# Kernel tuning notes

Measured on AMD Instinct MI355X. Metric: run time of the kernel, lower is better.

The kernel has to match this reference:

```python
import jax, jax.numpy as jnp
import numpy as np

HEADS = 4
DIM_HEAD = 32
GROUPS = 32  # min(256//4, 32)
EPS = 1e-5


def setup_inputs() -> dict:
    key = jax.random.key(0)
    ks = jax.random.split(key, 5)
    B, C, H, W = 16, 256, 64, 64
    CD, HC, WC = 512, 32, 32
    hid = HEADS * DIM_HEAD  # 128
    return {
        "x": jax.random.normal(ks[0], (B, C, H, W), jnp.float32),
        "cond": jax.random.normal(ks[1], (B, CD, HC, WC), jnp.float32),
        "gn_w": jnp.ones((C,), jnp.float32),
        "gn_b": jnp.zeros((C,), jnp.float32),
        "w_q": jax.random.normal(ks[2], (hid, C), jnp.float32) * 0.05,
        "b_q": jnp.zeros((hid,), jnp.float32),
        "w_kv": jax.random.normal(ks[3], (2 * hid, CD), jnp.float32) * 0.05,
        "b_kv": jnp.zeros((2 * hid,), jnp.float32),
        "w_out": jax.random.normal(ks[4], (C, hid), jnp.float32) * 0.05,
        "b_out": jnp.zeros((C,), jnp.float32),
    }


def _group_norm(x, w, b):
    # x: (B, C, H, W); normalize per group over (channels-in-group, H, W)
    B, C, H, W = x.shape
    xg = x.reshape(B, GROUPS, C // GROUPS, H, W)
    mu = jnp.mean(xg, axis=(2, 3, 4), keepdims=True)
    var = jnp.var(xg, axis=(2, 3, 4), keepdims=True)
    xn = ((xg - mu) * jax.lax.rsqrt(var + EPS)).reshape(B, C, H, W)
    return xn * w[None, :, None, None] + b[None, :, None, None]


def _conv1x1(x, w, b):
    # x: (B, Cin, H, W), w: (Cout, Cin), b: (Cout,)
    return jnp.einsum('oc,bchw->bohw', w, x) + b[None, :, None, None]


def reference(x, cond, gn_w, gn_b, w_q, b_q, w_kv, b_kv, w_out, b_out):
    B, C, H, W = x.shape
    hid = HEADS * DIM_HEAD
    xn = _group_norm(x, gn_w, gn_b)
    q = _conv1x1(xn, w_q, b_q)          # (B, hid, H, W)
    kv = _conv1x1(cond, w_kv, b_kv)     # (B, 2*hid, Hc, Wc)
    Nc = kv.shape[2] * kv.shape[3]
    N = H * W
    k = kv[:, :hid].reshape(B, HEADS, DIM_HEAD, Nc)
    v = kv[:, hid:].reshape(B, HEADS, DIM_HEAD, Nc)
    q = q.reshape(B, HEADS, DIM_HEAD, N)
    k = jax.nn.softmax(k, axis=-1)
    # kv outer product: (B, heads, d, e)
    context = jnp.einsum('bhdn,bhen->bhde', k, v)
    # query contraction over d: (B, heads, e, n)
    out = jnp.einsum('bhde,bhdn->bhen', context, q)
    out = out.reshape(B, hid, H, W)
    return _conv1x1(out, w_out, b_out)
```

## Files before the change

kernel.cpp:

```cpp
#include <hip/hip_runtime.h>
#include <hip/hip_bf16.h>

typedef __attribute__((ext_vector_type(8))) short bf16x8;
typedef __attribute__((ext_vector_type(4))) float f32x4;

__device__ __forceinline__ ushort f2bf(float f) {
    __hip_bfloat16 h = __float2bfloat16(f);
    return __builtin_bit_cast(ushort, h);
}
__device__ __forceinline__ unsigned pack2(float a, float b) {
    return (unsigned)f2bf(a) | ((unsigned)f2bf(b) << 16);
}
__device__ __forceinline__ float bflo(unsigned u) { return __uint_as_float(u << 16); }
__device__ __forceinline__ float bfhi(unsigned u) { return __uint_as_float(u & 0xffff0000u); }

__device__ __forceinline__ void unpack8(uint4 r, float* o) {
    o[0] = bflo(r.x); o[1] = bfhi(r.x); o[2] = bflo(r.y); o[3] = bfhi(r.y);
    o[4] = bflo(r.z); o[5] = bfhi(r.z); o[6] = bflo(r.w); o[7] = bfhi(r.w);
}

__global__ __launch_bounds__(256) void kv_gemm(const float* __restrict__ w_kv,
                                               const float* __restrict__ cond,
                                               const float* __restrict__ b_kv,
                                               ushort* __restrict__ kv16,
                                               float* __restrict__ zbase) {
    __shared__ ushort lA[128 * 64];
    __shared__ ushort lB[32 * 64];
    __shared__ float scratch[64 * 32];
    int nc = blockIdx.x, rb = blockIdx.y, b = blockIdx.z;
    int t = threadIdx.x;
    int fid = blockIdx.x + 32 * (blockIdx.y + 2 * blockIdx.z);
    if (fid < 264) zbase[fid * 256 + t] = 0.f;
    int col0 = nc * 32, row0 = rb * 128;
    int l = t & 63, w = t >> 6;
    int lr = l & 15, lg = l >> 4;
    const float* Ab32 = w_kv + (size_t)row0 * 512;
    const float* Bb = cond + (size_t)b * 512 * 1024 + col0;
    int rA = t >> 3, gAr = t & 7, gw = gAr ^ (rA & 7);
    int rB = t >> 3, gB = t & 7;
    int sp = t & 31, sj4 = (t >> 5) & 7;
    float4 ka0_, ka1_, ka2_, ka3_, ka4_, ka5_, ka6_, ka7_;
    float4 kb0_, kb1_;
#define KG_LOADA(k0) { \
    ka0_ = *(const float4*)&Ab32[(size_t)(rA)      * 512 + (k0) + gAr * 8]; \
    ka1_ = *(const float4*)&Ab32[(size_t)(rA)      * 512 + (k0) + gAr * 8 + 4]; \
    ka2_ = *(const float4*)&Ab32[(size_t)(32 + rA) * 512 + (k0) + gAr * 8]; \
    ka3_ = *(const float4*)&Ab32[(size_t)(32 + rA) * 512 + (k0) + gAr * 8 + 4]; \
    ka4_ = *(const float4*)&Ab32[(size_t)(64 + rA) * 512 + (k0) + gAr * 8]; \
    ka5_ = *(const float4*)&Ab32[(size_t)(64 + rA) * 512 + (k0) + gAr * 8 + 4]; \
    ka6_ = *(const float4*)&Ab32[(size_t)(96 + rA) * 512 + (k0) + gAr * 8]; \
    ka7_ = *(const float4*)&Ab32[(size_t)(96 + rA) * 512 + (k0) + gAr * 8 + 4]; }
#define KG_LOADB(k0) { \
    kb0_ = *(const float4*)&Bb[(size_t)((k0) + rB)      * 1024 + gB * 4]; \
    kb1_ = *(const float4*)&Bb[(size_t)((k0) + 32 + rB) * 1024 + gB * 4]; }
#define KG_WRITEA() { uint4 p; \
    p.x = pack2(ka0_.x, ka0_.y); p.y = pack2(ka0_.z, ka0_.w); \
    p.z = pack2(ka1_.x, ka1_.y); p.w = pack2(ka1_.z, ka1_.w); \
    *(uint4*)((char*)lA + (size_t)((rA)      * 8 + gw) * 16) = p; \
    p.x = pack2(ka2_.x, ka2_.y); p.y = pack2(ka2_.z, ka2_.w); \
    p.z = pack2(ka3_.x, ka3_.y); p.w = pack2(ka3_.z, ka3_.w); \
    *(uint4*)((char*)lA + (size_t)((32 + rA) * 8 + gw) * 16) = p; \
    p.x = pack2(ka4_.x, ka4_.y); p.y = pack2(ka4_.z, ka4_.w); \
    p.z = pack2(ka5_.x, ka5_.y); p.w = pack2(ka5_.z, ka5_.w); \
    *(uint4*)((char*)lA + (size_t)((64 + rA) * 8 + gw) * 16) = p; \
    p.x = pack2(ka6_.x, ka6_.y); p.y = pack2(ka6_.z, ka6_.w); \
    p.z = pack2(ka7_.x, ka7_.y); p.w = pack2(ka7_.z, ka7_.w); \
    *(uint4*)((char*)lA + (size_t)((96 + rA) * 8 + gw) * 16) = p; }
#define KG_WRITEB() { \
    *(float4*)((char*)scratch + (rB)      * 128 + ((gB ^ (((rB)      >> 1) & 7)) * 16)) = kb0_; \
    *(float4*)((char*)scratch + (32 + rB) * 128 + ((gB ^ (((32 + rB) >> 1) & 7)) * 16)) = kb1_; }
#define KG_PACKB() { \
    int js = sj4 ^ (sp & 7); \
    float4 s0 = *(const float4*)((char*)scratch + (2*sp)   * 128 + js * 16); \
    float4 s2 = *(const float4*)((char*)scratch + (2*sp+1) * 128 + js * 16); \
    float c0v[4] = {s0.x, s0.y, s0.z, s0.w}; \
    float c1v[4] = {s2.x, s2.y, s2.z, s2.w}; \
    _Pragma("unroll") \
    for (int w4 = 0; w4 < 4; ++w4) { \
        int n = sj4 * 4 + w4; \
        unsigned pk = pack2(c0v[w4], c1v[w4]); \
        *(unsigned*)((char*)lB + n * 128 + (((sp >> 2) ^ (n & 7)) * 16) + (sp & 3) * 4) = pk; \
    } }
    KG_LOADA(0); KG_LOADB(0);
    f32x4 acc[2][2] = {};
    for (int it = 0; it < 8; ++it) {
        KG_WRITEA();
        KG_WRITEB();
        __syncthreads();
        if (it < 7) { KG_LOADA(it * 64 + 64); KG_LOADB(it * 64 + 64); }
        KG_PACKB();
        __syncthreads();
        __builtin_amdgcn_s_setprio(1);
        #pragma unroll
        for (int ks = 0; ks < 2; ++ks) {
            bf16x8 av[2], bv[2];
            #pragma unroll
            for (int mi = 0; mi < 2; ++mi) {
                int ar = w * 32 + mi * 16 + lr;
                int q = (ks * 4 + lg) ^ (ar & 7);
                av[mi] = *(const bf16x8*)((const char*)lA + ar * 128 + q * 16);
            }
            #pragma unroll
            for (int ni = 0; ni < 2; ++ni) {
                int br = ni * 16 + lr;
                int q = (ks * 4 + lg) ^ (br & 7);
                bv[ni] = *(const bf16x8*)((const char*)lB + br * 128 + q * 16);
            }
            #pragma unroll
            for (int mi = 0; mi < 2; ++mi)
                #pragma unroll
                for (int ni = 0; ni < 2; ++ni)
                    acc[mi][ni] = __builtin_amdgcn_mfma_f32_16x16x32_bf16(
                        av[mi], bv[ni], acc[mi][ni], 0, 0, 0);
        }
        __builtin_amdgcn_s_setprio(0);
        __syncthreads();
    }
#undef KG_LOADA
#undef KG_LOADB
#undef KG_WRITEA
#undef KG_WRITEB
#undef KG_PACKB
    int orow = row0 + w * 32;
    #pragma unroll
    for (int mi = 0; mi < 2; ++mi) {
        int rbase = orow + mi * 16 + lg * 4;
        float4 b4 = *(const float4*)&b_kv[rbase];
        float bvr[4] = {b4.x, b4.y, b4.z, b4.w};
        #pragma unroll
        for (int ni = 0; ni < 2; ++ni) {
            int cc = col0 + ni * 16 + lr;
            #pragma unroll
            for (int r = 0; r < 4; ++r)
                kv16[((size_t)b * 256 + rbase + r) * 1024 + cc] = f2bf(acc[mi][ni][r] + bvr[r]);
        }
    }
}

__global__ __launch_bounds__(256) void ctxstats_kernel(const ushort* __restrict__ kv,
                                                       const float* __restrict__ x,
                                                       float* __restrict__ rowsum,
                                                       float* __restrict__ ctx,
                                                       float* __restrict__ statacc) {
    __shared__ float pl[32][129], vl[32][129];
    int bid = blockIdx.x, t = threadIdx.x;
    if (bid < 512) {
        int bh = bid >> 3, b = bh >> 2, h = bh & 3;
        int n0 = (bid & 7) * 128;
        int r = t >> 3, cs = (t & 7) * 16;
        const ushort* kp = kv + ((size_t)b * 256 + h * 32 + r) * 1024 + n0 + cs;
        const ushort* vp = kv + ((size_t)b * 256 + 128 + h * 32 + r) * 1024 + n0 + cs;
        float kvals[16], vvals[16];
        unpack8(((const uint4*)kp)[0], kvals);
        unpack8(((const uint4*)kp)[1], kvals + 8);
        unpack8(((const uint4*)vp)[0], vvals);
        unpack8(((const uint4*)vp)[1], vvals + 8);
        float psum = 0.f;
        #pragma unroll
        for (int i = 0; i < 16; ++i) {
            float e = __expf(kvals[i]);
            pl[r][cs + i] = e;
            vl[r][cs + i] = vvals[i];
            psum += e;
        }
        psum += __shfl_xor(psum, 1, 64);
        psum += __shfl_xor(psum, 2, 64);
        psum += __shfl_xor(psum, 4, 64);
        if ((t & 7) == 0) atomicAdd(&rowsum[bh * 32 + r], psum);
        __syncthreads();
        int d0 = t >> 5, e0 = t & 31;
        float acc[4] = {0.f, 0.f, 0.f, 0.f};
        #pragma unroll 8
        for (int nn = 0; nn < 128; ++nn) {
            float vv = vl[e0][nn];
            #pragma unroll
            for (int i = 0; i < 4; ++i)
                acc[i] += pl[d0 + 8 * i][nn] * vv;
        }
        #pragma unroll
        for (int i = 0; i < 4; ++i)
            atomicAdd(&ctx[((size_t)bh * 32 + d0 + 8 * i) * 32 + e0], acc[i]);
    } else {
        int bg = bid - 512;
        const float4* xp = (const float4*)(x + (size_t)bg * 32768);
        float s = 0.f, ss = 0.f;
        #pragma unroll
        for (int j = 0; j < 32; ++j) {
            float4 v = xp[t + 256 * j];
            s  += v.x + v.y + v.z + v.w;
            ss += v.x*v.x + v.y*v.y + v.z*v.z + v.w*v.w;
        }
        #pragma unroll
        for (int off = 32; off > 0; off >>= 1) {
            s  += __shfl_down(s, off, 64);
            ss += __shfl_down(ss, off, 64);
        }
        int wave = t >> 6;
        if ((t & 63) == 0) { pl[0][wave * 2] = s; pl[0][wave * 2 + 1] = ss; }
        __syncthreads();
        if (t == 0) {
            statacc[bg * 2]     = pl[0][0] + pl[0][2] + pl[0][4] + pl[0][6];
            statacc[bg * 2 + 1] = pl[0][1] + pl[0][3] + pl[0][5] + pl[0][7];
        }
    }
}

__global__ __launch_bounds__(256) void a_kernel(const float* __restrict__ ctx,
                                                const float* __restrict__ rowsum,
                                                const float* __restrict__ w_out,
                                                const float* __restrict__ w_q,
                                                const float* __restrict__ b_q,
                                                const float* __restrict__ b_out,
                                                ushort* __restrict__ A16,
                                                float* __restrict__ biasb) {
    __shared__ float ctxl[4][32][33];
    __shared__ float wol[16][128];
    __shared__ float ml[16][128];
    int b = blockIdx.x >> 4, ot = (blockIdx.x & 15) << 4;
    int t = threadIdx.x;
    #pragma unroll
    for (int j = 0; j < 16; ++j) {
        int e = t + 256 * j;
        float inv = 1.f / rowsum[b * 128 + (e >> 5)];
        ctxl[e >> 10][(e >> 5) & 31][e & 31] = ctx[(size_t)b * 4096 + e] * inv;
    }
    #pragma unroll
    for (int j = 0; j < 8; ++j) {
        int e = t + 256 * j;
        wol[e >> 7][e & 127] = w_out[(ot + (e >> 7)) * 128 + (e & 127)];
    }
    __syncthreads();
    #pragma unroll
    for (int j = 0; j < 8; ++j) {
        int e = t + 256 * j;
        int o = e >> 7, hd = e & 127, h = hd >> 5, d = hd & 31;
        float acc = 0.f;
        #pragma unroll
        for (int ee = 0; ee < 32; ++ee) acc += wol[o][h * 32 + ee] * ctxl[h][d][ee];
        ml[o][hd] = acc;
    }
    __syncthreads();
    int c = t;
    float wt[16];
    #pragma unroll
    for (int o = 0; o < 16; ++o) wt[o] = 0.f;
    for (int hd = 0; hd < 128; ++hd) {
        float wq = w_q[hd * 256 + c];
        #pragma unroll
        for (int o = 0; o < 16; ++o) wt[o] += ml[o][hd] * wq;
    }
    ushort* Abp = A16 + ((size_t)b * 256 + ot) * 256 + c;
    #pragma unroll
    for (int o = 0; o < 16; ++o)
        Abp[(size_t)o * 256] = f2bf(wt[o]);
    if (t < 16) {
        int o = t;
        float md = 0.f;
        #pragma unroll 8
        for (int hd = 0; hd < 128; ++hd) md += ml[o][hd] * b_q[hd];
        biasb[(size_t)b * 256 + ot + o] = md + b_out[ot + o];
    }
}

__global__ __launch_bounds__(512) void out_gemm_fused(const ushort* __restrict__ A16,
                                                      const float* __restrict__ x,
                                                      const float* __restrict__ statacc,
                                                      const float* __restrict__ gn_w,
                                                      const float* __restrict__ gn_b,
                                                      const float* __restrict__ biasb,
                                                      float* __restrict__ out) {
    __shared__ ushort lA[256 * 64];
    __shared__ ushort lB[64 * 64];
    __shared__ float scratch[64 * 64];
    __shared__ float sct[256][2];
    int b = blockIdx.y;
    int n0 = blockIdx.x * 64;
    int t = threadIdx.x;
    int l = t & 63, wid = t >> 6;
    int wr = wid >> 1, wc = wid & 1;
    int lr = l & 15, lg = l >> 4;
    const ushort* Ab = A16 + (size_t)b * 65536;
    const float* xb = x + (size_t)b * 256 * 4096 + n0;
    int sp = t & 31, sj4 = t >> 5;
    if (t < 256) {
        int g = t >> 3;
        float S  = statacc[(b * 32 + g) * 2];
        float SS = statacc[(b * 32 + g) * 2 + 1];
        float mu  = S * (1.f / 32768.f);
        float var = SS * (1.f / 32768.f) - mu * mu;
        float sc = rsqrtf(var + 1e-5f) * gn_w[t];
        sct[t][0] = sc;
        sct[t][1] = gn_b[t] - mu * sc;
    }
    uint4 a0_, a1_, a2_, a3_;
    float4 b0_, b1_;
    int rA = t >> 3, gA = (t & 7) ^ (rA & 7);
    int rB = t >> 4, gB = t & 15;
#define OG_LOADA(k0) { \
    a0_ = *(const uint4*)(Ab + (size_t)(rA)       * 256 + (k0) + gA * 8); \
    a1_ = *(const uint4*)(Ab + (size_t)(64 + rA)  * 256 + (k0) + gA * 8); \
    a2_ = *(const uint4*)(Ab + (size_t)(128 + rA) * 256 + (k0) + gA * 8); \
    a3_ = *(const uint4*)(Ab + (size_t)(192 + rA) * 256 + (k0) + gA * 8); }
#define OG_LOADB(k0) { \
    b0_ = *(const float4*)&xb[(size_t)((k0) + rB)      * 4096 + gB * 4]; \
    b1_ = *(const float4*)&xb[(size_t)((k0) + 32 + rB) * 4096 + gB * 4]; }
    OG_LOADA(0); OG_LOADB(0);
    f32x4 acc[4][2] = {};
    for (int it = 0; it < 4; ++it) {
        int k0 = it * 64;
        *(uint4*)((char*)lA + (size_t)t * 16)          = a0_;
        *(uint4*)((char*)lA + (size_t)(512 + t) * 16)  = a1_;
        *(uint4*)((char*)lA + (size_t)(1024 + t) * 16) = a2_;
        *(uint4*)((char*)lA + (size_t)(1536 + t) * 16) = a3_;
        *(float4*)((char*)scratch + (rB)      * 256 + ((gB ^ (((rB)      >> 1) & 15)) * 16)) = b0_;
        *(float4*)((char*)scratch + (32 + rB) * 256 + ((gB ^ (((32 + rB) >> 1) & 15)) * 16)) = b1_;
        __syncthreads();
        if (it < 3) { OG_LOADA(k0 + 64); OG_LOADB(k0 + 64); }
        {
            int js = sj4 ^ (sp & 15);
            float sc0 = sct[k0 + 2 * sp][0],     tc0 = sct[k0 + 2 * sp][1];
            float sc1 = sct[k0 + 2 * sp + 1][0], tc1 = sct[k0 + 2 * sp + 1][1];
            float4 s0 = *(const float4*)((char*)scratch + (2*sp)   * 256 + js * 16);
            float4 s2 = *(const float4*)((char*)scratch + (2*sp+1) * 256 + js * 16);
            float c0v[4] = {s0.x, s0.y, s0.z, s0.w};
            float c1v[4] = {s2.x, s2.y, s2.z, s2.w};
            #pragma unroll
            for (int w4 = 0; w4 < 4; ++w4) {
                int n = sj4 * 4 + w4;
                unsigned pk = pack2(c0v[w4] * sc0 + tc0, c1v[w4] * sc1 + tc1);
                *(unsigned*)((char*)lB + n * 128 + (((sp >> 2) ^ (n & 7)) * 16) + (sp & 3) * 4) = pk;
            }
        }
        __syncthreads();
        __builtin_amdgcn_s_setprio(1);
        #pragma unroll
        for (int ks = 0; ks < 2; ++ks) {
            bf16x8 av[4], bv[2];
            #pragma unroll
            for (int mi = 0; mi < 4; ++mi) {
                int ar = wr * 64 + mi * 16 + lr;
                int q = (ks * 4 + lg) ^ (ar & 7);
                av[mi] = *(const bf16x8*)((const char*)lA + ar * 128 + q * 16);
            }
            #pragma unroll
            for (int ni = 0; ni < 2; ++ni) {
                int br = wc * 32 + ni * 16 + lr;
                int q = (ks * 4 + lg) ^ (br & 7);
                bv[ni] = *(const bf16x8*)((const char*)lB + br * 128 + q * 16);
            }
            #pragma unroll
            for (int mi = 0; mi < 4; ++mi)
                #pragma unroll
                for (int ni = 0; ni < 2; ++ni)
                    acc[mi][ni] = __builtin_amdgcn_mfma_f32_16x16x32_bf16(
                        av[mi], bv[ni], acc[mi][ni], 0, 0, 0);
        }
        __builtin_amdgcn_s_setprio(0);
        __syncthreads();
    }
#undef OG_LOADA
#undef OG_LOADB
    const float* bp = biasb + (size_t)b * 256;
    int orow = wr * 64, ocol = n0 + wc * 32 + lr;
    #pragma unroll
    for (int mi = 0; mi < 4; ++mi) {
        int rb2 = orow + mi * 16 + lg * 4;
        float4 b4 = *(const float4*)&bp[rb2];
        float bvr[4] = {b4.x, b4.y, b4.z, b4.w};
        #pragma unroll
        for (int ni = 0; ni < 2; ++ni) {
            int cc = ocol + ni * 16;
            #pragma unroll
            for (int r = 0; r < 4; ++r)
                out[((size_t)b * 256 + rb2 + r) * 4096 + cc] = acc[mi][ni][r] + bvr[r];
        }
    }
}

extern "C" void kernel_launch(void* const* d_in, const int* in_sizes, int n_in,
                              void* d_out, int out_size, void* d_ws, size_t ws_size,
                              hipStream_t stream) {
    const float* x     = (const float*)d_in[0];
    const float* cond  = (const float*)d_in[1];
    const float* gn_w  = (const float*)d_in[2];
    const float* gn_b  = (const float*)d_in[3];
    const float* w_q   = (const float*)d_in[4];
    const float* b_q   = (const float*)d_in[5];
    const float* w_kv  = (const float*)d_in[6];
    const float* b_kv  = (const float*)d_in[7];
    const float* w_out = (const float*)d_in[8];
    const float* b_out = (const float*)d_in[9];
    float* out = (float*)d_out;

    float* f       = (float*)d_ws;
    float* statacc = f;
    float* rowsum  = f + 1024;
    float* ctx     = f + 3072;
    float* biasb   = f + 68608;
    ushort* u      = (ushort*)(f + 72704);
    ushort* kv16   = u;
    ushort* A16    = u + 4194304;

    kv_gemm<<<dim3(32, 2, 16), 256, 0, stream>>>(w_kv, cond, b_kv, kv16, rowsum);
    ctxstats_kernel<<<1024, 256, 0, stream>>>(kv16, x, rowsum, ctx, statacc);
    a_kernel<<<256, 256, 0, stream>>>(ctx, rowsum, w_out, w_q, b_q, b_out, A16, biasb);
    out_gemm_fused<<<dim3(64, 16), 512, 0, stream>>>(A16, x, statacc, gn_w, gn_b, biasb, out);
}
```

Measured before the change: 78.80 us.

## Load weight MFMA fragments directly from global memory instead of staging through LDS

In both the KV GEMM and the output GEMM, the A-operand (weights) is no longer copied into shared memory. Each lane now loads its MFMA fragment straight from global memory into registers, converting to bf16 on the fly for the KV weights. This removes the LDS writes and reads for A and shrinks shared memory use, which may allow higher occupancy. In exchange, the A loads are no longer prefetched one iteration ahead, so their latency sits between the barriers, and the global access pattern is less coalesced and is repeated by every block.

New measurement: 111.0 us. +40.8%, slower.

```diff
diff --git a/kernel.cpp b/kernel.cpp
--- a/kernel.cpp
+++ b/kernel.cpp
@@ -17,6 +17,12 @@
 __device__ __forceinline__ void unpack8(uint4 r, float* o) {
     o[0] = bflo(r.x); o[1] = bfhi(r.x); o[2] = bflo(r.y); o[3] = bfhi(r.y);
     o[4] = bflo(r.z); o[5] = bfhi(r.z); o[6] = bflo(r.w); o[7] = bfhi(r.w);
+}
+__device__ __forceinline__ bf16x8 cvt8(float4 u0, float4 u1) {
+    uint4 p;
+    p.x = pack2(u0.x, u0.y); p.y = pack2(u0.z, u0.w);
+    p.z = pack2(u1.x, u1.y); p.w = pack2(u1.z, u1.w);
+    return __builtin_bit_cast(bf16x8, p);
 }
 
 __global__ __launch_bounds__(256) void kv_gemm(const float* __restrict__ w_kv,
@@ -24,7 +30,6 @@
                                                const float* __restrict__ b_kv,
                                                ushort* __restrict__ kv16,
                                                float* __restrict__ zbase) {
-    __shared__ ushort lA[128 * 64];
     __shared__ ushort lB[32 * 64];
     __shared__ float scratch[64 * 32];
     int nc = blockIdx.x, rb = blockIdx.y, b = blockIdx.z;
@@ -34,38 +39,22 @@
     int col0 = nc * 32, row0 = rb * 128;
     int l = t & 63, w = t >> 6;
     int lr = l & 15, lg = l >> 4;
-    const float* Ab32 = w_kv + (size_t)row0 * 512;
     const float* Bb = cond + (size_t)b * 512 * 1024 + col0;
-    int rA = t >> 3, gAr = t & 7, gw = gAr ^ (rA & 7);
+    const float* Ar0 = w_kv + (size_t)(row0 + w * 32 + lr) * 512;
+    const float* Ar1 = w_kv + (size_t)(row0 + w * 32 + 16 + lr) * 512;
+    int kq0 = lg * 8, kq1 = (4 + lg) * 8;
     int rB = t >> 3, gB = t & 7;
     int sp = t & 31, sj4 = (t >> 5) & 7;
-    float4 ka0_, ka1_, ka2_, ka3_, ka4_, ka5_, ka6_, ka7_;
     float4 kb0_, kb1_;
-#define KG_LOADA(k0) { \
-    ka0_ = *(const float4*)&Ab32[(size_t)(rA)      * 512 + (k0) + gAr * 8]; \
-    ka1_ = *(const float4*)&Ab32[(size_t)(rA)      * 512 + (k0) + gAr * 8 + 4]; \
-    ka2_ = *(const float4*)&Ab32[(size_t)(32 + rA) * 512 + (k0) + gAr * 8]; \
-    ka3_ = *(const float4*)&Ab32[(size_t)(32 + rA) * 512 + (k0) + gAr * 8 + 4]; \
-    ka4_ = *(const float4*)&Ab32[(size_t)(64 + rA) * 512 + (k0) + gAr * 8]; \
-    ka5_ = *(const float4*)&Ab32[(size_t)(64 + rA) * 512 + (k0) + gAr * 8 + 4]; \
-    ka6_ = *(const float4*)&Ab32[(size_t)(96 + rA) * 512 + (k0) + gAr * 8]; \
-    ka7_ = *(const float4*)&Ab32[(size_t)(96 + rA) * 512 + (k0) + gAr * 8 + 4]; }
+    bf16x8 af00_, af01_, af10_, af11_;
 #define KG_LOADB(k0) { \
     kb0_ = *(const float4*)&Bb[(size_t)((k0) + rB)      * 1024 + gB * 4]; \
     kb1_ = *(const float4*)&Bb[(size_t)((k0) + 32 + rB) * 1024 + gB * 4]; }
-#define KG_WRITEA() { uint4 p; \
-    p.x = pack2(ka0_.x, ka0_.y); p.y = pack2(ka0_.z, ka0_.w); \
-    p.z = pack2(ka1_.x, ka1_.y); p.w = pack2(ka1_.z, ka1_.w); \
-    *(uint4*)((char*)lA + (size_t)((rA)      * 8 + gw) * 16) = p; \
-    p.x = pack2(ka2_.x, ka2_.y); p.y = pack2(ka2_.z, ka2_.w); \
-    p.z = pack2(ka3_.x, ka3_.y); p.w = pack2(ka3_.z, ka3_.w); \
-    *(uint4*)((char*)lA + (size_t)((32 + rA) * 8 + gw) * 16) = p; \
-    p.x = pack2(ka4_.x, ka4_.y); p.y = pack2(ka4_.z, ka4_.w); \
-    p.z = pack2(ka5_.x, ka5_.y); p.w = pack2(ka5_.z, ka5_.w); \
-    *(uint4*)((char*)lA + (size_t)((64 + rA) * 8 + gw) * 16) = p; \
-    p.x = pack2(ka6_.x, ka6_.y); p.y = pack2(ka6_.z, ka6_.w); \
-    p.z = pack2(ka7_.x, ka7_.y); p.w = pack2(ka7_.z, ka7_.w); \
-    *(uint4*)((char*)lA + (size_t)((96 + rA) * 8 + gw) * 16) = p; }
+#define KG_LOADAF(k0) { \
+    af00_ = cvt8(*(const float4*)&Ar0[(k0) + kq0], *(const float4*)&Ar0[(k0) + kq0 + 4]); \
+    af01_ = cvt8(*(const float4*)&Ar0[(k0) + kq1], *(const float4*)&Ar0[(k0) + kq1 + 4]); \
+    af10_ = cvt8(*(const float4*)&Ar1[(k0) + kq0], *(const float4*)&Ar1[(k0) + kq0 + 4]); \
+    af11_ = cvt8(*(const float4*)&Ar1[(k0) + kq1], *(const float4*)&Ar1[(k0) + kq1 + 4]); }
 #define KG_WRITEB() { \
     *(float4*)((char*)scratch + (rB)      * 128 + ((gB ^ (((rB)      >> 1) & 7)) * 16)) = kb0_; \
     *(float4*)((char*)scratch + (32 + rB) * 128 + ((gB ^ (((32 + rB) >> 1) & 7)) * 16)) = kb1_; }
@@ -81,44 +70,42 @@
         unsigned pk = pack2(c0v[w4], c1v[w4]); \
         *(unsigned*)((char*)lB + n * 128 + (((sp >> 2) ^ (n & 7)) * 16) + (sp & 3) * 4) = pk; \
     } }
-    KG_LOADA(0); KG_LOADB(0);
-    f32x4 acc[2][2] = {};
+    KG_LOADB(0);
+    f32x4 acc00 = {}, acc01 = {}, acc10 = {}, acc11 = {};
     for (int it = 0; it < 8; ++it) {
-        KG_WRITEA();
+        int k0 = it * 64;
         KG_WRITEB();
         __syncthreads();
-        if (it < 7) { KG_LOADA(it * 64 + 64); KG_LOADB(it * 64 + 64); }
+        if (it < 7) KG_LOADB(k0 + 64);
+        KG_LOADAF(k0);
         KG_PACKB();
         __syncthreads();
         __builtin_amdgcn_s_setprio(1);
-        #pragma unroll
-        for (int ks = 0; ks < 2; ++ks) {
-            bf16x8 av[2], bv[2];
-            #pragma unroll
-            for (int mi = 0; mi < 2; ++mi) {
-                int ar = w * 32 + mi * 16 + lr;
-                int q = (ks * 4 + lg) ^ (ar & 7);
-                av[mi] = *(const bf16x8*)((const char*)lA + ar * 128 + q * 16);
-            }
-            #pragma unroll
-            for (int ni = 0; ni < 2; ++ni) {
-                int br = ni * 16 + lr;
-                int q = (ks * 4 + lg) ^ (br & 7);
-                bv[ni] = *(const bf16x8*)((const char*)lB + br * 128 + q * 16);
-            }
-            #pragma unroll
-            for (int mi = 0; mi < 2; ++mi)
-                #pragma unroll
-                for (int ni = 0; ni < 2; ++ni)
-                    acc[mi][ni] = __builtin_amdgcn_mfma_f32_16x16x32_bf16(
-                        av[mi], bv[ni], acc[mi][ni], 0, 0, 0);
+        {
+            int br0 = lr,      q0 = lg ^ (br0 & 7);
+            int br1 = 16 + lr, q1 = lg ^ (br1 & 7);
+            bf16x8 bv0 = *(const bf16x8*)((const char*)lB + br0 * 128 + q0 * 16);
+            bf16x8 bv1 = *(const bf16x8*)((const char*)lB + br1 * 128 + q1 * 16);
+            acc00 = __builtin_amdgcn_mfma_f32_16x16x32_bf16(af00_, bv0, acc00, 0, 0, 0);
+            acc01 = __builtin_amdgcn_mfma_f32_16x16x32_bf16(af00_, bv1, acc01, 0, 0, 0);
+            acc10 = __builtin_amdgcn_mfma_f32_16x16x32_bf16(af10_, bv0, acc10, 0, 0, 0);
+            acc11 = __builtin_amdgcn_mfma_f32_16x16x32_bf16(af10_, bv1, acc11, 0, 0, 0);
+        }
+        {
+            int br0 = lr,      q0 = (4 + lg) ^ (br0 & 7);
+            int br1 = 16 + lr, q1 = (4 + lg) ^ (br1 & 7);
+            bf16x8 bv0 = *(const bf16x8*)((const char*)lB + br0 * 128 + q0 * 16);
+            bf16x8 bv1 = *(const bf16x8*)((const char*)lB + br1 * 128 + q1 * 16);
+            acc00 = __builtin_amdgcn_mfma_f32_16x16x32_bf16(af01_, bv0, acc00, 0, 0, 0);
+            acc01 = __builtin_amdgcn_mfma_f32_16x16x32_bf16(af01_, bv1, acc01, 0, 0, 0);
+            acc10 = __builtin_amdgcn_mfma_f32_16x16x32_bf16(af11_, bv0, acc10, 0, 0, 0);
+            acc11 = __builtin_amdgcn_mfma_f32_16x16x32_bf16(af11_, bv1, acc11, 0, 0, 0);
         }
         __builtin_amdgcn_s_setprio(0);
         __syncthreads();
     }
-#undef KG_LOADA
 #undef KG_LOADB
-#undef KG_WRITEA
+#undef KG_LOADAF
 #undef KG_WRITEB
 #undef KG_PACKB
     int orow = row0 + w * 32;
@@ -127,12 +114,12 @@
         int rbase = orow + mi * 16 + lg * 4;
         float4 b4 = *(const float4*)&b_kv[rbase];
         float bvr[4] = {b4.x, b4.y, b4.z, b4.w};
-        #pragma unroll
-        for (int ni = 0; ni < 2; ++ni) {
-            int cc = col0 + ni * 16 + lr;
-            #pragma unroll
-            for (int r = 0; r < 4; ++r)
-                kv16[((size_t)b * 256 + rbase + r) * 1024 + cc] = f2bf(acc[mi][ni][r] + bvr[r]);
+        f32x4 a0 = mi == 0 ? acc00 : acc10;
+        f32x4 a1 = mi == 0 ? acc01 : acc11;
+        #pragma unroll
+        for (int r = 0; r < 4; ++r) {
+            kv16[((size_t)b * 256 + rbase + r) * 1024 + col0 + lr]      = f2bf(a0[r] + bvr[r]);
+            kv16[((size_t)b * 256 + rbase + r) * 1024 + col0 + 16 + lr] = f2bf(a1[r] + bvr[r]);
         }
     }
 }
@@ -269,7 +256,6 @@
                                                       const float* __restrict__ gn_b,
                                                       const float* __restrict__ biasb,
                                                       float* __restrict__ out) {
-    __shared__ ushort lA[256 * 64];
     __shared__ ushort lB[64 * 64];
     __shared__ float scratch[64 * 64];
     __shared__ float sct[256][2];
@@ -292,30 +278,31 @@
         sct[t][0] = sc;
         sct[t][1] = gn_b[t] - mu * sc;
     }
-    uint4 a0_, a1_, a2_, a3_;
+    const ushort* ArA = Ab + (size_t)(wr * 64 + lr) * 256;
+    const ushort* ArB = Ab + (size_t)(wr * 64 + 16 + lr) * 256;
+    const ushort* ArC = Ab + (size_t)(wr * 64 + 32 + lr) * 256;
+    const ushort* ArD = Ab + (size_t)(wr * 64 + 48 + lr) * 256;
+    int kq0 = lg * 8, kq1 = (4 + lg) * 8;
     float4 b0_, b1_;
-    int rA = t >> 3, gA = (t & 7) ^ (rA & 7);
+    bf16x8 af0a_, af0b_, af1a_, af1b_, af2a_, af2b_, af3a_, af3b_;
     int rB = t >> 4, gB = t & 15;
-#define OG_LOADA(k0) { \
-    a0_ = *(const uint4*)(Ab + (size_t)(rA)       * 256 + (k0) + gA * 8); \
-    a1_ = *(const uint4*)(Ab + (size_t)(64 + rA)  * 256 + (k0) + gA * 8); \
-    a2_ = *(const uint4*)(Ab + (size_t)(128 + rA) * 256 + (k0) + gA * 8); \
-    a3_ = *(const uint4*)(Ab + (size_t)(192 + rA) * 256 + (k0) + gA * 8); }
 #define OG_LOADB(k0) { \
     b0_ = *(const float4*)&xb[(size_t)((k0) + rB)      * 4096 + gB * 4]; \
     b1_ = *(const float4*)&xb[(size_t)((k0) + 32 + rB) * 4096 + gB * 4]; }
-    OG_LOADA(0); OG_LOADB(0);
+#define OG_LOADAF(k0) { \
+    af0a_ = *(const bf16x8*)(ArA + (k0) + kq0); af0b_ = *(const bf16x8*)(ArA + (k0) + kq1); \
+    af1a_ = *(const bf16x8*)(ArB + (k0) + kq0); af1b_ = *(const bf16x8*)(ArB + (k0) + kq1); \
+    af2a_ = *(const bf16x8*)(ArC + (k0) + kq0); af2b_ = *(const bf16x8*)(ArC + (k0) + kq1); \
+    af3a_ = *(const bf16x8*)(ArD + (k0) + kq0); af3b_ = *(const bf16x8*)(ArD + (k0) + kq1); }
+    OG_LOADB(0);
     f32x4 acc[4][2] = {};
     for (int it = 0; it < 4; ++it) {
         int k0 = it * 64;
-        *(uint4*)((char*)lA + (size_t)t * 16)          = a0_;
-        *(uint4*)((char*)lA + (size_t)(512 + t) * 16)  = a1_;
-        *(uint4*)((char*)lA + (size_t)(1024 + t) * 16) = a2_;
-        *(uint4*)((char*)lA + (size_t)(1536 + t) * 16) = a3_;
         *(float4*)((char*)scratch + (rB)      * 256 + ((gB ^ (((rB)      >> 1) & 15)) * 16)) = b0_;
         *(float4*)((char*)scratch + (32 + rB) * 256 + ((gB ^ (((32 + rB) >> 1) & 15)) * 16)) = b1_;
         __syncthreads();
-        if (it < 3) { OG_LOADA(k0 + 64); OG_LOADB(k0 + 64); }
+        if (it < 3) OG_LOADB(k0 + 64);
+        OG_LOADAF(k0);
         {
             int js = sj4 ^ (sp & 15);
             float sc0 = sct[k0 + 2 * sp][0],     tc0 = sct[k0 + 2 * sp][1];
@@ -333,33 +320,39 @@
         }
         __syncthreads();
         __builtin_amdgcn_s_setprio(1);
-        #pragma unroll
-        for (int ks = 0; ks < 2; ++ks) {
-            bf16x8 av[4], bv[2];
-            #pragma unroll
-            for (int mi = 0; mi < 4; ++mi) {
-                int ar = wr * 64 + mi * 16 + lr;
-                int q = (ks * 4 + lg) ^ (ar & 7);
-                av[mi] = *(const bf16x8*)((const char*)lA + ar * 128 + q * 16);
-            }
-            #pragma unroll
-            for (int ni = 0; ni < 2; ++ni) {
-                int br = wc * 32 + ni * 16 + lr;
-                int q = (ks * 4 + lg) ^ (br & 7);
-                bv[ni] = *(const bf16x8*)((const char*)lB + br * 128 + q * 16);
-            }
-            #pragma unroll
-            for (int mi = 0; mi < 4; ++mi)
-                #pragma unroll
-                for (int ni = 0; ni < 2; ++ni)
-                    acc[mi][ni] = __builtin_amdgcn_mfma_f32_16x16x32_bf16(
-                        av[mi], bv[ni], acc[mi][ni], 0, 0, 0);
+        {
+            int br0 = wc * 32 + lr,      q0 = lg ^ (br0 & 7);
+            int br1 = wc * 32 + 16 + lr, q1 = lg ^ (br1 & 7);
+            bf16x8 bv0 = *(const bf16x8*)((const char*)lB + br0 * 128 + q0 * 16);
+            bf16x8 bv1 = *(const bf16x8*)((const char*)lB + br1 * 128 + q1 * 16);
+            acc[0][0] = __builtin_amdgcn_mfma_f32_16x16x32_bf16(af0a_, bv0, acc[0][0], 0, 0, 0);
+            acc[0][1] = __builtin_amdgcn_mfma_f32_16x16x32_bf16(af0a_, bv1, acc[0][1], 0, 0, 0);
+            acc[1][0] = __builtin_amdgcn_mfma_f32_16x16x32_bf16(af1a_, bv0, acc[1][0], 0, 0, 0);
+            acc[1][1] = __builtin_amdgcn_mfma_f32_16x16x32_bf16(af1a_, bv1, acc[1][1], 0, 0, 0);
+            acc[2][0] = __builtin_amdgcn_mfma_f32_16x16x32_bf16(af2a_, bv0, acc[2][0], 0, 0, 0);
+            acc[2][1] = __builtin_amdgcn_mfma_f32_16x16x32_bf16(af2a_, bv1, acc[2][1], 0, 0, 0);
+            acc[3][0] = __builtin_amdgcn_mfma_f32_16x16x32_bf16(af3a_, bv0, acc[3][0], 0, 0, 0);
+            acc[3][1] = __builtin_amdgcn_mfma_f32_16x16x32_bf16(af3a_, bv1, acc[3][1], 0, 0, 0);
+        }
+        {
+            int br0 = wc * 32 + lr,      q0 = (4 + lg) ^ (br0 & 7);
+            int br1 = wc * 32 + 16 + lr, q1 = (4 + lg) ^ (br1 & 7);
+            bf16x8 bv0 = *(const bf16x8*)((const char*)lB + br0 * 128 + q0 * 16);
+            bf16x8 bv1 = *(const bf16x8*)((const char*)lB + br1 * 128 + q1 * 16);
+            acc[0][0] = __builtin_amdgcn_mfma_f32_16x16x32_bf16(af0b_, bv0, acc[0][0], 0, 0, 0);
+            acc[0][1] = __builtin_amdgcn_mfma_f32_16x16x32_bf16(af0b_, bv1, acc[0][1], 0, 0, 0);
+            acc[1][0] = __builtin_amdgcn_mfma_f32_16x16x32_bf16(af1b_, bv0, acc[1][0], 0, 0, 0);
+            acc[1][1] = __builtin_amdgcn_mfma_f32_16x16x32_bf16(af1b_, bv1, acc[1][1], 0, 0, 0);
+            acc[2][0] = __builtin_amdgcn_mfma_f32_16x16x32_bf16(af2b_, bv0, acc[2][0], 0, 0, 0);
+            acc[2][1] = __builtin_amdgcn_mfma_f32_16x16x32_bf16(af2b_, bv1, acc[2][1], 0, 0, 0);
+            acc[3][0] = __builtin_amdgcn_mfma_f32_16x16x32_bf16(af3b_, bv0, acc[3][0], 0, 0, 0);
+            acc[3][1] = __builtin_amdgcn_mfma_f32_16x16x32_bf16(af3b_, bv1, acc[3][1], 0, 0, 0);
         }
         __builtin_amdgcn_s_setprio(0);
         __syncthreads();
     }
-#undef OG_LOADA
 #undef OG_LOADB
+#undef OG_LOADAF
     const float* bp = biasb + (size_t)b * 256;
     int orow = wr * 64, ocol = n0 + wc * 32 + lr;
     #pragma unroll
```
